# Kernel tuning notes

Hardware: AMD Instinct MI355X
Metric: run time of the kernel (lower is better)

Reference implementation:

```python
import jax, jax.numpy as jnp
import numpy as np

KSIZE = 3; STRIDE = 1; RATE = 2; FUSE_K = 3; SCALE = 10.0; EPS = 1e-4
B, C, RH, RW = 2, 128, 80, 80  # raw (full-res) feature shape


def setup_inputs() -> dict:
    key = jax.random.key(0)
    ks = jax.random.split(key, 5)
    shp = (B, C, RH, RW)
    names = ["left", "right", "mid", "raw_left", "raw_right"]
    return {n: jax.random.normal(k, shp, dtype=jnp.float32) for n, k in zip(names, ks)}


def _same_pads(H, W, k, s):
    oh, ow = -(-H // s), -(-W // s)
    ph = max(0, (oh - 1) * s + k - H)
    pw = max(0, (ow - 1) * s + k - W)
    return ((ph // 2, ph - ph // 2), (pw // 2, pw - pw // 2))


def extract_patches(x, k, s):
    # torch extract_image_patches with 'same' padding -> (b, L, c, k, k)
    b, c, H, W = x.shape
    pads = _same_pads(H, W, k, s)
    p = jax.lax.conv_general_dilated_patches(x, (k, k), (s, s), pads)  # (b, c*k*k, oh, ow)
    oh, ow = p.shape[2], p.shape[3]
    p = p.reshape(b, c, k, k, oh * ow)  # feature dim is channel-major (c, k, k), like torch unfold
    return p.transpose(0, 4, 1, 2, 3)


def _fuse(s, Hl, Wl, Hm, Wm):
    # diagonal fuse-conv: conv of (b,1,L,P) score image with eye(k), twice with transposes
    b = s.shape[0]
    k = FUSE_K
    eye = jnp.eye(k, dtype=s.dtype).reshape(1, 1, k, k)
    pad = ((k // 2, k // 2), (k // 2, k // 2))
    conv = lambda x: jax.lax.conv_general_dilated(x, eye, (1, 1), pad)
    x = conv(s.reshape(b, 1, Hl * Wl, Hm * Wm))
    x = x.reshape(b, Hl, Wl, Hm, Wm).transpose(0, 2, 1, 4, 3).reshape(b, 1, Wl * Hl, Wm * Hm)
    x = conv(x)
    x = x.reshape(b, Wl, Hl, Wm, Hm).transpose(0, 2, 1, 4, 3)  # (b, Hl, Wl, Hm, Wm)
    return x.reshape(b, Hl * Wl, Hm, Wm)


def _deconv_one(attn, patches):
    # torch conv_transpose2d(attn, patches, stride=RATE, padding=1):
    # conv with lhs dilation RATE, spatially-flipped kernel, padding k-1-1
    kk = patches.shape[-1]
    rhs = jnp.flip(patches, (-2, -1)).transpose(1, 0, 2, 3)  # (C, L, kk, kk)
    p = kk - 1 - 1
    out = jax.lax.conv_general_dilated(attn[None], rhs, (1, 1), ((p, p), (p, p)),
                                       lhs_dilation=(RATE, RATE),
                                       dimension_numbers=('NCHW', 'OIHW', 'NCHW'))
    return out[0]


def _forward(left, right, mid, raw_left, raw_right):
    kernel = 2 * RATE
    rawp_l = extract_patches(raw_left, kernel, RATE * STRIDE)   # (B, L, C, 4, 4)
    rawp_r = extract_patches(raw_right, kernel, RATE * STRIDE)
    # nearest downsample by rate
    l = left[:, :, ::RATE, ::RATE]
    r = right[:, :, ::RATE, ::RATE]
    m = mid[:, :, ::RATE, ::RATE]
    Hl, Wl = l.shape[2], l.shape[3]
    Hm, Wm = m.shape[2], m.shape[3]
    lp = extract_patches(l, KSIZE, STRIDE)   # (B, L, C, 3, 3)
    rp = extract_patches(r, KSIZE, STRIDE)
    mp = extract_patches(m, KSIZE, STRIDE)   # (B, P, C, 3, 3); conv2d(same-padded xi, w) == patch dot

    def norm(p):
        # torch: sqrt(reduce_sum(p^2 + eps)) -- eps added elementwise before the sum
        return p / jnp.sqrt(jnp.sum(p * p + EPS, axis=(2, 3, 4), keepdims=True))

    sl = jnp.einsum('bqcij,bpcij->bqp', norm(lp), mp).reshape(-1, Hl * Wl, Hm, Wm)
    sr = jnp.einsum('bqcij,bpcij->bqp', norm(rp), mp).reshape(-1, Hl * Wl, Hm, Wm)
    sl = _fuse(sl, Hl, Wl, Hm, Wm)
    sr = _fuse(sr, Hl, Wl, Hm, Wm)
    al = jax.nn.softmax(sl * SCALE, axis=1)
    ar = jax.nn.softmax(sr * SCALE, axis=1)
    y_l = jax.vmap(_deconv_one)(al, rawp_l) / 4.0   # (B, C, RH, RW)
    y_r = jax.vmap(_deconv_one)(ar, rawp_r) / 4.0
    # cos_function_weight: cosine blending ramp along width (1 at left edge -> 0 at right edge)
    w = 0.5 * (1.0 + jnp.cos(jnp.pi * jnp.arange(RW, dtype=y_l.dtype) / (RW - 1)))
    w = w.reshape(1, 1, 1, RW)
    return w * y_l + jnp.flip(w, 3) * y_r


def reference(left, right, mid, raw_left, raw_right):
    return _forward(left, right, mid, raw_left, raw_right)
```

## Files before the change

kernel.cpp:

```cpp
#include <hip/hip_runtime.h>
#include <hip/hip_bf16.h>

typedef __hip_bfloat16 bf16;
typedef __attribute__((ext_vector_type(8))) short short8;
typedef __attribute__((ext_vector_type(4))) float f32x4;
typedef unsigned short ushort_t;

#define PI_F 3.14159265358979323846f
#define GPAD_Z 3111696L

#define GLOAD_LDS16(gp, lp)                                                    \
  __builtin_amdgcn_global_load_lds(                                            \
      (const __attribute__((address_space(1))) unsigned int*)(gp),             \
      (__attribute__((address_space(3))) unsigned int*)(lp), 16, 0, 0)

__global__ __launch_bounds__(128) void prep_pt(const float* __restrict__ left,
                                               const float* __restrict__ right,
                                               const float* __restrict__ mid,
                                               bf16* __restrict__ PTe,
                                               bf16* __restrict__ MTe,
                                               float* __restrict__ SQ) {
  int q = blockIdx.x;
  int y = blockIdx.y;
  int c = threadIdx.x;
  int qi = q / 40, qj = q - qi * 40;
  const float* src;
  bf16* dst;
  int b;
  bool aside = (y < 4);
  if (aside) {
    b = y & 1;
    src = (y < 2) ? left : right;
    dst = PTe + (long)y * 1664 * 384;
  } else {
    b = y - 4;
    src = mid;
    dst = MTe + (long)(y - 4) * 1664 * 384;
  }
  float v = src[(((long)b * 128 + c) * 80 + 2 * qi) * 80 + 2 * qj];
  bf16 hi = __float2bfloat16(v);
  bf16 lo = __float2bfloat16(v - __bfloat162float(hi));
  if (aside) {
    dst[(long)q * 384 + c] = hi;
    dst[(long)q * 384 + 128 + c] = lo;
    dst[(long)q * 384 + 256 + c] = hi;
  } else {
    dst[(long)q * 384 + c] = hi;
    dst[(long)q * 384 + 128 + c] = hi;
    dst[(long)q * 384 + 256 + c] = lo;
  }
  if (aside) {
    __shared__ float red[128];
    red[c] = v * v;
    __syncthreads();
    for (int s = 64; s > 0; s >>= 1) {
      if (c < s) red[c] += red[c + s];
      __syncthreads();
    }
    if (c == 0) SQ[y * 1600 + q] = red[0];
  }
}

__global__ void invn_kernel(const float* __restrict__ SQ, float* __restrict__ INV) {
  int idx = blockIdx.x * 256 + threadIdx.x;
  if (idx >= 6400) return;
  int z = idx / 1600, q = idx - z * 1600;
  int qi = q / 40, qj = q - qi * 40;
  float s = 0.1152f;
  #pragma unroll
  for (int di = -1; di <= 1; ++di)
    #pragma unroll
    for (int dj = -1; dj <= 1; ++dj) {
      int a = qi + di, b = qj + dj;
      if (a >= 0 && a < 40 && b >= 0 && b < 40) s += SQ[z * 1600 + a * 40 + b];
    }
  INV[idx] = rsqrtf(s);
}

__global__ __launch_bounds__(256) void gemm_nt(const bf16* __restrict__ A,
                                               const bf16* __restrict__ B,
                                               float* __restrict__ C,
                                               int M, int N, int K,
                                               long Az, long Bz, long Cz,
                                               int bmod, int cpad) {
  int z = blockIdx.z;
  A += (long)z * Az;
  B += (long)(bmod ? (z & 1) : z) * Bz;
  C += (long)z * Cz;
  __shared__ bf16 As[128 * 32];
  __shared__ bf16 Bs[128 * 32];
  int lane = threadIdx.x & 63;
  int w = threadIdx.x >> 6;
  int mb = blockIdx.x * 128;
  int nb = blockIdx.y * 128;
  int lr = lane >> 2;
  int gb = (lane & 3) ^ ((lane >> 3) & 3);
  int lm = lane & 15;
  int swz = (lm >> 1) & 3;
  int kb = lane >> 4;
  int pos = (kb ^ swz) * 8;
  int warow = (w >> 1) * 64;
  int wbrow = (w & 1) * 64;
  f32x4 acc[4][4];
  #pragma unroll
  for (int i = 0; i < 4; ++i)
    #pragma unroll
    for (int j = 0; j < 4; ++j) {
      f32x4 zv = {0.f, 0.f, 0.f, 0.f};
      acc[i][j] = zv;
    }
  for (int k0 = 0; k0 < K; k0 += 32) {
    __syncthreads();
    #pragma unroll
    for (int t = 0; t < 2; ++t) {
      int r = (w * 2 + t) * 16 + lr;
      GLOAD_LDS16(A + (long)(mb + r) * K + k0 + gb * 8, As + (w * 2 + t) * 512);
      GLOAD_LDS16(B + (long)(nb + r) * K + k0 + gb * 8, Bs + (w * 2 + t) * 512);
    }
    __syncthreads();
    short8 af[4], bfr[4];
    #pragma unroll
    for (int i = 0; i < 4; ++i) {
      af[i]  = *reinterpret_cast<const short8*>(As + (warow + i * 16 + lm) * 32 + pos);
      bfr[i] = *reinterpret_cast<const short8*>(Bs + (wbrow + i * 16 + lm) * 32 + pos);
    }
    #pragma unroll
    for (int i = 0; i < 4; ++i)
      #pragma unroll
      for (int j = 0; j < 4; ++j)
        acc[i][j] = __builtin_amdgcn_mfma_f32_16x16x32_bf16(af[i], bfr[j], acc[i][j], 0, 0, 0);
  }
  int m0 = mb + warow;
  int n0 = nb + wbrow;
  int col = lane & 15;
  int r0 = (lane >> 4) * 4;
  #pragma unroll
  for (int i = 0; i < 4; ++i)
    #pragma unroll
    for (int j = 0; j < 4; ++j) {
      int n = n0 + j * 16 + col;
      if (n < N) {
        int nc = cpad ? ((n / 40) * 42 + (n - (n / 40) * 40) + 43) : n;
        #pragma unroll
        for (int r = 0; r < 4; ++r) {
          int m = m0 + i * 16 + r0 + r;
          if (m < M) {
            long mr = cpad ? ((long)((m / 40) * 42 + (m - (m / 40) * 40) + 43) * 1764)
                           : ((long)m * N);
            C[mr + nc] = acc[i][j][r];
          }
        }
      }
    }
}

__global__ __launch_bounds__(256) void s1fuse1_kernel(const float* __restrict__ Gp,
                                                      const float* __restrict__ INV,
                                                      float* __restrict__ S2) {
  int p = blockIdx.x * 256 + threadIdx.x;
  if (p >= 1600) return;
  int q = blockIdx.y, z = blockIdx.z;
  const float* Gz = Gp + (long)z * GPAD_Z;
  float s = 0.f;
  #pragma unroll
  for (int d = -1; d <= 1; ++d) {
    int q2 = q + d, p2 = p + d;
    bool ok = ((unsigned)q2 < 1600u) && ((unsigned)p2 < 1600u);
    int q2c = ok ? q2 : 0;
    int p2c = ok ? p2 : 0;
    float wgt = ok ? INV[z * 1600 + q2c] : 0.f;
    int qi = q2c / 40, qj = q2c - qi * 40;
    int pi = p2c / 40, pj = p2c - pi * 40;
    const float* base = Gz + (long)(qi * 42 + qj + 43) * 1764 + (pi * 42 + pj + 43);
    float t = 0.f;
    #pragma unroll
    for (int di = -1; di <= 1; ++di)
      #pragma unroll
      for (int dj = -1; dj <= 1; ++dj)
        t += base[(long)(di * 42 + dj) * 1765];
    s += t * wgt;
  }
  S2[((long)z * 1600 + q) * 1600 + p] = s;
}

__global__ __launch_bounds__(256) void fuse2_kernel(const float* __restrict__ S2,
                                                    float* __restrict__ S3) {
  int p = blockIdx.x * 256 + threadIdx.x;
  if (p >= 1600) return;
  int q = blockIdx.y, z = blockIdx.z;
  const float* S = S2 + (long)z * 2560000;
  int il = q / 40, jl = q - il * 40;
  int im = p / 40, jm = p - im * 40;
  int u = jl * 40 + il, v = jm * 40 + im;
  float s = 0.f;
  #pragma unroll
  for (int d = -1; d <= 1; ++d) {
    int u2 = u + d, v2 = v + d;
    if (u2 >= 0 && u2 < 1600 && v2 >= 0 && v2 < 1600) {
      int q2 = (u2 % 40) * 40 + u2 / 40;
      int p2 = (v2 % 40) * 40 + v2 / 40;
      s += S[(long)q2 * 1600 + p2];
    }
  }
  S3[((long)z * 1600 + q) * 1600 + p] = s;
}

__global__ __launch_bounds__(256) void smax_part(const float* __restrict__ S3,
                                                 float* __restrict__ Pm,
                                                 float* __restrict__ Ps) {
  int z = blockIdx.z, qc = blockIdx.y;
  int pl = threadIdx.x & 63;
  int ql = threadIdx.x >> 6;
  int p = blockIdx.x * 64 + pl;
  const float* S = S3 + (long)z * 2560000;
  float m = -1e30f, s = 0.f;
  for (int i = 0; i < 50; ++i) {
    int q = qc * 200 + i * 4 + ql;
    float x = 10.f * S[(long)q * 1600 + p];
    if (x > m) { s *= __expf(m - x); m = x; }
    s += __expf(x - m);
  }
  __shared__ float lm[4][64], ls[4][64];
  lm[ql][pl] = m;
  ls[ql][pl] = s;
  __syncthreads();
  if (ql == 0) {
    float M = m, SS = s;
    #pragma unroll
    for (int j = 1; j < 4; ++j) {
      float mj = lm[j][pl], sj = ls[j][pl];
      if (mj > M) { SS = SS * __expf(M - mj) + sj; M = mj; }
      else SS += sj * __expf(mj - M);
    }
    Pm[((long)z * 8 + qc) * 1600 + p] = M;
    Ps[((long)z * 8 + qc) * 1600 + p] = SS;
  }
}

__global__ void smax_comb(const float* __restrict__ Pm, const float* __restrict__ Ps,
                          float* __restrict__ Fm, float* __restrict__ Fs) {
  int idx = blockIdx.x * 256 + threadIdx.x;
  if (idx >= 6400) return;
  int z = idx / 1600, p = idx - z * 1600;
  float M = -1e30f;
  #pragma unroll
  for (int c = 0; c < 8; ++c) M = fmaxf(M, Pm[((long)z * 8 + c) * 1600 + p]);
  float S = 0.f;
  #pragma unroll
  for (int c = 0; c < 8; ++c)
    S += Ps[((long)z * 8 + c) * 1600 + p] * __expf(Pm[((long)z * 8 + c) * 1600 + p] - M);
  Fm[idx] = M;
  Fs[idx] = 1.f / S;
}

__global__ __launch_bounds__(256) void smax_write(const float* __restrict__ S3,
                                                  const float* __restrict__ Fm,
                                                  const float* __restrict__ Fs,
                                                  bf16* __restrict__ AT) {
  int z = blockIdx.z;
  int p0 = blockIdx.x * 64, q0 = blockIdx.y * 64;
  int pl = threadIdx.x & 63, ql = threadIdx.x >> 6;
  __shared__ ushort_t T[64][66];
  float fm = Fm[z * 1600 + p0 + pl];
  float fs = Fs[z * 1600 + p0 + pl];
  const float* S = S3 + (long)z * 2560000;
  #pragma unroll
  for (int i = 0; i < 16; ++i) {
    int qq = ql + i * 4;
    float x = 10.f * S[(long)(q0 + qq) * 1600 + p0 + pl];
    bf16 h = __float2bfloat16(__expf(x - fm) * fs);
    T[pl][qq] = *reinterpret_cast<ushort_t*>(&h);
  }
  __syncthreads();
  int rp = threadIdx.x >> 5;
  int j = threadIdx.x & 31;
  #pragma unroll
  for (int pass = 0; pass < 8; ++pass) {
    int row = pass * 8 + rp;
    unsigned int vv = (unsigned int)T[row][2 * j] | ((unsigned int)T[row][2 * j + 1] << 16);
    *reinterpret_cast<unsigned int*>(AT + ((long)z * 1664 + p0 + row) * 1600 + q0 + 2 * j) = vv;
  }
}

__global__ __launch_bounds__(256) void rawpt_kernel(const float* __restrict__ rawL,
                                                    const float* __restrict__ rawR,
                                                    bf16* __restrict__ RAWPT) {
  int z = blockIdx.z;
  int r = blockIdx.y * 4 + (threadIdx.x >> 6);
  int q = blockIdx.x * 64 + (threadIdx.x & 63);
  const float* raw = ((z < 2) ? rawL : rawR) + (long)(z & 1) * 819200;
  int c = r >> 4, i = (r >> 2) & 3, j = r & 3;
  int qi = q / 40, qj = q - qi * 40;
  int y = 2 * qi + i - 1, x = 2 * qj + j - 1;
  float v = 0.f;
  if (y >= 0 && y < 80 && x >= 0 && x < 80) v = raw[((long)c * 80 + y) * 80 + x];
  RAWPT[((long)z * 2048 + r) * 1600 + q] = __float2bfloat16(v);
}

__global__ __launch_bounds__(256) void paste_kernel(const float* __restrict__ Z,
                                                    float* __restrict__ out) {
  int idx = blockIdx.x * 256 + threadIdx.x;
  int x = idx % 80;
  int t = idx / 80;
  int y = t % 80;
  t /= 80;
  int c = t % 128;
  int b = t / 128;
  int imA = (y - 1) >> 1, ipA = y - 2 * imA + 1;
  int jmA = (x - 1) >> 1, jpA = x - 2 * jmA + 1;
  const long zs = 2048L * 1600;
  const float* ZL = Z + (long)b * zs;
  const float* ZR = Z + (long)(2 + b) * zs;
  float aL = 0.f, aR = 0.f;
  #pragma unroll
  for (int a = 0; a < 2; ++a) {
    int im = imA + a, ip = ipA - 2 * a;
    if (im < 0 || im > 39) continue;
    #pragma unroll
    for (int e = 0; e < 2; ++e) {
      int jm = jmA + e, jp = jpA - 2 * e;
      if (jm < 0 || jm > 39) continue;
      long off = (long)((c << 4) + ip * 4 + jp) * 1600 + im * 40 + jm;
      aL += ZL[off];
      aR += ZR[off];
    }
  }
  float wx = 0.5f * (1.f + cosf(PI_F * x / 79.f));
  float wf = 0.5f * (1.f + cosf(PI_F * (79 - x) / 79.f));
  out[idx] = 0.25f * (wx * aL + wf * aR);
}

extern "C" void kernel_launch(void* const* d_in, const int* in_sizes, int n_in,
                              void* d_out, int out_size, void* d_ws, size_t ws_size,
                              hipStream_t stream) {
  const float* left  = (const float*)d_in[0];
  const float* right = (const float*)d_in[1];
  const float* mid   = (const float*)d_in[2];
  const float* rawL  = (const float*)d_in[3];
  const float* rawR  = (const float*)d_in[4];
  float* out = (float*)d_out;
  char* ws = (char*)d_ws;

  bf16*  PTe   = (bf16*)(ws + 0);
  bf16*  MTe   = (bf16*)(ws + 5111808);
  float* SQ    = (float*)(ws + 7667712);
  float* INV   = (float*)(ws + 7693312);
  float* Pm    = (float*)(ws + 7718912);
  float* Ps    = (float*)(ws + 7923712);
  float* Fm    = (float*)(ws + 8128512);
  float* Fs    = (float*)(ws + 8154112);
  float* X     = (float*)(ws + 8179712);
  float* Y     = (float*)(ws + 60608512);
  bf16*  AT    = (bf16*)(ws + 101568512);
  bf16*  RAWPT = (bf16*)Y;

  prep_pt<<<dim3(1600, 6, 1), 128, 0, stream>>>(left, right, mid, PTe, MTe, SQ);
  invn_kernel<<<25, 256, 0, stream>>>(SQ, INV);
  hipMemsetAsync(X, 0, (size_t)4 * GPAD_Z * sizeof(float), stream);
  gemm_nt<<<dim3(13, 13, 4), 256, 0, stream>>>(PTe, MTe, X, 1600, 1600, 384,
                                               1664L * 384, 1664L * 384, GPAD_Z, 1, 1);
  s1fuse1_kernel<<<dim3(7, 1600, 4), 256, 0, stream>>>(X, INV, Y);
  fuse2_kernel<<<dim3(7, 1600, 4), 256, 0, stream>>>(Y, X);
  smax_part<<<dim3(25, 8, 4), 256, 0, stream>>>(X, Pm, Ps);
  smax_comb<<<25, 256, 0, stream>>>(Pm, Ps, Fm, Fs);
  smax_write<<<dim3(25, 25, 4), 256, 0, stream>>>(X, Fm, Fs, AT);
  rawpt_kernel<<<dim3(25, 512, 4), 256, 0, stream>>>(rawL, rawR, RAWPT);
  gemm_nt<<<dim3(16, 13, 4), 256, 0, stream>>>(RAWPT, AT, X, 2048, 1600, 1600,
                                               2048L * 1600, 1664L * 1600, 2048L * 1600, 0, 0);
  paste_kernel<<<6400, 256, 0, stream>>>(X, out);
}
```

Baseline: 358.6 us.

## Fuse second diagonal conv into softmax partials, widen GEMM K-tile, zero only pad border

Merges the second fuse-conv pass into the softmax partial-reduction kernel, so the fused score is written once and reduced in the same pass instead of being re-read by a separate kernel. The GEMM K-tile grows from 32 to 64 with a new XOR swizzle over 8 chunks, halving loop iterations and barriers at the cost of more LDS. The full memset of the padded score buffer is replaced with a kernel that zeros only the border rows and columns the GEMM leaves unwritten. The fused kernel runs on far fewer blocks (25x8x4), so the stencil work loses parallelism.

Measured after the change: 371.7 us. +3.6%, slower.

```diff
diff --git a/kernel.cpp b/kernel.cpp
--- a/kernel.cpp
+++ b/kernel.cpp
@@ -77,6 +77,21 @@
   INV[idx] = rsqrtf(s);
 }
 
+__global__ __launch_bounds__(256) void padzero_kernel(float* __restrict__ Gp) {
+  int row = blockIdx.x;
+  int z = blockIdx.y;
+  float* R = Gp + (long)z * GPAD_Z + (long)row * 1764;
+  int r42 = row % 42;
+  if (r42 == 0 || r42 == 41) {
+    for (int c = threadIdx.x; c < 1764; c += 256) R[c] = 0.f;
+  } else {
+    for (int i = threadIdx.x; i < 84; i += 256) {
+      int c = (i >> 1) * 42 + ((i & 1) ? 41 : 0);
+      R[c] = 0.f;
+    }
+  }
+}
+
 __global__ __launch_bounds__(256) void gemm_nt(const bf16* __restrict__ A,
                                                const bf16* __restrict__ B,
                                                float* __restrict__ C,
@@ -87,18 +102,17 @@
   A += (long)z * Az;
   B += (long)(bmod ? (z & 1) : z) * Bz;
   C += (long)z * Cz;
-  __shared__ bf16 As[128 * 32];
-  __shared__ bf16 Bs[128 * 32];
+  __shared__ bf16 As[128 * 64];
+  __shared__ bf16 Bs[128 * 64];
   int lane = threadIdx.x & 63;
   int w = threadIdx.x >> 6;
   int mb = blockIdx.x * 128;
   int nb = blockIdx.y * 128;
-  int lr = lane >> 2;
-  int gb = (lane & 3) ^ ((lane >> 3) & 3);
+  int lr8 = lane >> 3;
+  int gb8 = (lane & 7) ^ (lr8 & 7);
   int lm = lane & 15;
-  int swz = (lm >> 1) & 3;
   int kb = lane >> 4;
-  int pos = (kb ^ swz) * 8;
+  int lms = lm & 7;
   int warow = (w >> 1) * 64;
   int wbrow = (w & 1) * 64;
   f32x4 acc[4][4];
@@ -109,26 +123,31 @@
       f32x4 zv = {0.f, 0.f, 0.f, 0.f};
       acc[i][j] = zv;
     }
-  for (int k0 = 0; k0 < K; k0 += 32) {
+  for (int k0 = 0; k0 < K; k0 += 64) {
     __syncthreads();
     #pragma unroll
-    for (int t = 0; t < 2; ++t) {
-      int r = (w * 2 + t) * 16 + lr;
-      GLOAD_LDS16(A + (long)(mb + r) * K + k0 + gb * 8, As + (w * 2 + t) * 512);
-      GLOAD_LDS16(B + (long)(nb + r) * K + k0 + gb * 8, Bs + (w * 2 + t) * 512);
+    for (int t = 0; t < 4; ++t) {
+      int r = w * 32 + t * 8 + lr8;
+      GLOAD_LDS16(A + (long)(mb + r) * K + k0 + gb8 * 8, As + (w * 32 + t * 8) * 64);
+      GLOAD_LDS16(B + (long)(nb + r) * K + k0 + gb8 * 8, Bs + (w * 32 + t * 8) * 64);
     }
     __syncthreads();
-    short8 af[4], bfr[4];
-    #pragma unroll
-    for (int i = 0; i < 4; ++i) {
-      af[i]  = *reinterpret_cast<const short8*>(As + (warow + i * 16 + lm) * 32 + pos);
-      bfr[i] = *reinterpret_cast<const short8*>(Bs + (wbrow + i * 16 + lm) * 32 + pos);
-    }
-    #pragma unroll
-    for (int i = 0; i < 4; ++i)
+    #pragma unroll
+    for (int kk8 = 0; kk8 < 8; kk8 += 4) {
+      short8 af[4], bfr[4];
       #pragma unroll
-      for (int j = 0; j < 4; ++j)
-        acc[i][j] = __builtin_amdgcn_mfma_f32_16x16x32_bf16(af[i], bfr[j], acc[i][j], 0, 0, 0);
+      for (int i = 0; i < 4; ++i) {
+        af[i]  = *reinterpret_cast<const short8*>(
+            As + (warow + i * 16 + lm) * 64 + (((kb + kk8) ^ lms) * 8));
+        bfr[i] = *reinterpret_cast<const short8*>(
+            Bs + (wbrow + i * 16 + lm) * 64 + (((kb + kk8) ^ lms) * 8));
+      }
+      #pragma unroll
+      for (int i = 0; i < 4; ++i)
+        #pragma unroll
+        for (int j = 0; j < 4; ++j)
+          acc[i][j] = __builtin_amdgcn_mfma_f32_16x16x32_bf16(af[i], bfr[j], acc[i][j], 0, 0, 0);
+    }
   }
   int m0 = mb + warow;
   int n0 = nb + wbrow;
@@ -183,52 +202,47 @@
   S2[((long)z * 1600 + q) * 1600 + p] = s;
 }
 
-__global__ __launch_bounds__(256) void fuse2_kernel(const float* __restrict__ S2,
-                                                    float* __restrict__ S3) {
-  int p = blockIdx.x * 256 + threadIdx.x;
-  if (p >= 1600) return;
-  int q = blockIdx.y, z = blockIdx.z;
-  const float* S = S2 + (long)z * 2560000;
-  int il = q / 40, jl = q - il * 40;
-  int im = p / 40, jm = p - im * 40;
-  int u = jl * 40 + il, v = jm * 40 + im;
-  float s = 0.f;
-  #pragma unroll
-  for (int d = -1; d <= 1; ++d) {
-    int u2 = u + d, v2 = v + d;
-    if (u2 >= 0 && u2 < 1600 && v2 >= 0 && v2 < 1600) {
-      int q2 = (u2 % 40) * 40 + u2 / 40;
-      int p2 = (v2 % 40) * 40 + v2 / 40;
-      s += S[(long)q2 * 1600 + p2];
-    }
-  }
-  S3[((long)z * 1600 + q) * 1600 + p] = s;
-}
-
-__global__ __launch_bounds__(256) void smax_part(const float* __restrict__ S3,
-                                                 float* __restrict__ Pm,
-                                                 float* __restrict__ Ps) {
+__global__ __launch_bounds__(256) void fuse2s_kernel(const float* __restrict__ S2,
+                                                     float* __restrict__ S3,
+                                                     float* __restrict__ Pm,
+                                                     float* __restrict__ Ps) {
   int z = blockIdx.z, qc = blockIdx.y;
   int pl = threadIdx.x & 63;
   int ql = threadIdx.x >> 6;
   int p = blockIdx.x * 64 + pl;
-  const float* S = S3 + (long)z * 2560000;
+  const float* S = S2 + (long)z * 2560000;
+  float* S3z = S3 + (long)z * 2560000;
+  int im = p / 40, jm = p - im * 40;
+  int v = jm * 40 + im;
   float m = -1e30f, s = 0.f;
   for (int i = 0; i < 50; ++i) {
     int q = qc * 200 + i * 4 + ql;
-    float x = 10.f * S[(long)q * 1600 + p];
+    int il = q / 40, jl = q - il * 40;
+    int u = jl * 40 + il;
+    float t = 0.f;
+    #pragma unroll
+    for (int d = -1; d <= 1; ++d) {
+      int u2 = u + d, v2 = v + d;
+      if ((unsigned)u2 < 1600u && (unsigned)v2 < 1600u) {
+        int q2 = (u2 % 40) * 40 + u2 / 40;
+        int p2 = (v2 % 40) * 40 + v2 / 40;
+        t += S[(long)q2 * 1600 + p2];
+      }
+    }
+    S3z[(long)q * 1600 + p] = t;
+    float x = 10.f * t;
     if (x > m) { s *= __expf(m - x); m = x; }
     s += __expf(x - m);
   }
-  __shared__ float lm[4][64], ls[4][64];
-  lm[ql][pl] = m;
-  ls[ql][pl] = s;
+  __shared__ float lm_[4][64], ls_[4][64];
+  lm_[ql][pl] = m;
+  ls_[ql][pl] = s;
   __syncthreads();
   if (ql == 0) {
     float M = m, SS = s;
     #pragma unroll
     for (int j = 1; j < 4; ++j) {
-      float mj = lm[j][pl], sj = ls[j][pl];
+      float mj = lm_[j][pl], sj = ls_[j][pl];
       if (mj > M) { SS = SS * __expf(M - mj) + sj; M = mj; }
       else SS += sj * __expf(mj - M);
     }
@@ -356,12 +370,11 @@
 
   prep_pt<<<dim3(1600, 6, 1), 128, 0, stream>>>(left, right, mid, PTe, MTe, SQ);
   invn_kernel<<<25, 256, 0, stream>>>(SQ, INV);
-  hipMemsetAsync(X, 0, (size_t)4 * GPAD_Z * sizeof(float), stream);
+  padzero_kernel<<<dim3(1764, 4), 256, 0, stream>>>(X);
   gemm_nt<<<dim3(13, 13, 4), 256, 0, stream>>>(PTe, MTe, X, 1600, 1600, 384,
                                                1664L * 384, 1664L * 384, GPAD_Z, 1, 1);
   s1fuse1_kernel<<<dim3(7, 1600, 4), 256, 0, stream>>>(X, INV, Y);
-  fuse2_kernel<<<dim3(7, 1600, 4), 256, 0, stream>>>(Y, X);
-  smax_part<<<dim3(25, 8, 4), 256, 0, stream>>>(X, Pm, Ps);
+  fuse2s_kernel<<<dim3(25, 8, 4), 256, 0, stream>>>(Y, X, Pm, Ps);
   smax_comb<<<25, 256, 0, stream>>>(Pm, Ps, Fm, Fs);
   smax_write<<<dim3(25, 25, 4), 256, 0, stream>>>(X, Fm, Fs, AT);
   rawpt_kernel<<<dim3(25, 512, 4), 256, 0, stream>>>(rawL, rawR, RAWPT);
```
